# Optimization experiments

Measured on AMD Instinct MI355X. Metric: run time of the kernel, lower is better.

## Reference

```python
import jax, jax.numpy as jnp
import numpy as np

N_POINTS = 2_000_000
DIM_FEAT = 32
GRID_H, GRID_W = 1024, 1024


def setup_inputs() -> dict:
    key = jax.random.key(0)
    k1, k2 = jax.random.split(key)
    # normalized coords in [-1, 1], grid_sample convention: coord[:,0]=x (W axis), coord[:,1]=y (H axis)
    coord = jax.random.uniform(k1, (N_POINTS, 2), dtype=jnp.float32, minval=-1.0, maxval=1.0)
    # learned feature grid [1, C, H, W] (original inits zeros; use randn for a non-trivial test)
    params = jax.random.normal(k2, (1, DIM_FEAT, GRID_H, GRID_W), dtype=jnp.float32)
    return {"coord": coord, "params": params}


def _grid_sample_2d(params, coord):
    """Bilinear grid_sample, align_corners=True, border-clamped corners.

    params: [1, C, H, W]; coord: [N, 2] in [-1, 1]. Returns [N, C].
    """
    C, H, W = params.shape[1], params.shape[2], params.shape[3]
    x, y = coord[:, 0], coord[:, 1]
    # unnormalize (align_corners=True)
    ix = (x + 1.0) * 0.5 * (W - 1)
    iy = (y + 1.0) * 0.5 * (H - 1)
    ix0 = jnp.floor(ix)
    iy0 = jnp.floor(iy)
    ix1 = ix0 + 1.0
    iy1 = iy0 + 1.0
    # bilinear weights (computed before index clamping)
    w_nw = (ix1 - ix) * (iy1 - iy)
    w_ne = (ix - ix0) * (iy1 - iy)
    w_sw = (ix1 - ix) * (iy - iy0)
    w_se = (ix - ix0) * (iy - iy0)
    # clamped integer corner indices
    ix0c = jnp.clip(ix0, 0, W - 1).astype(jnp.int32)
    ix1c = jnp.clip(ix1, 0, W - 1).astype(jnp.int32)
    iy0c = jnp.clip(iy0, 0, H - 1).astype(jnp.int32)
    iy1c = jnp.clip(iy1, 0, H - 1).astype(jnp.int32)
    p = params[0]  # [C, H, W]
    # gather 4 corners -> each [C, N]
    v_nw = p[:, iy0c, ix0c]
    v_ne = p[:, iy0c, ix1c]
    v_sw = p[:, iy1c, ix0c]
    v_se = p[:, iy1c, ix1c]
    out = v_nw * w_nw + v_ne * w_ne + v_sw * w_sw + v_se * w_se  # [C, N]
    return out.T  # [N, C]


def reference(coord, params):
    return _grid_sample_2d(params, coord)
```

## Files before the change

### kernel.cpp

```cpp
#include <hip/hip_runtime.h>

constexpr int N_POINTS = 2000000;
constexpr int C = 32;
constexpr int H = 1024;
constexpr int W = 1024;

typedef float f32x4 __attribute__((ext_vector_type(4)));
typedef float f32x2 __attribute__((ext_vector_type(2)));

__global__ __launch_bounds__(256) void transpose_chw_hwc(
    const float* __restrict__ in, float* __restrict__ out)
{
    __shared__ float tile[64][C + 1];
    const int x0  = blockIdx.x * 64;
    const int y   = blockIdx.y;
    const int tid = threadIdx.x;

#pragma unroll
    for (int r = 0; r < 2; ++r) {
        const int idx = tid + 256 * r;
        const int c   = idx >> 4;
        const int xq  = idx & 15;
        const f32x4 v = __builtin_nontemporal_load(
            (const f32x4*)&in[(size_t)c * (H * W) + (size_t)y * W + x0 + xq * 4]);
        tile[xq * 4 + 0][c] = v.x;
        tile[xq * 4 + 1][c] = v.y;
        tile[xq * 4 + 2][c] = v.z;
        tile[xq * 4 + 3][c] = v.w;
    }
    __syncthreads();

#pragma unroll
    for (int r = 0; r < 2; ++r) {
        const int idx = tid + 256 * r;
        const int x   = idx >> 3;
        const int c4  = idx & 7;
        f32x4 v;
        v.x = tile[x][c4 * 4 + 0];
        v.y = tile[x][c4 * 4 + 1];
        v.z = tile[x][c4 * 4 + 2];
        v.w = tile[x][c4 * 4 + 3];
        *(f32x4*)&out[((size_t)y * W + x0 + x) * C + c4 * 4] = v;
    }
}

__global__ __launch_bounds__(256) void sample_hwc(
    const float* __restrict__ coord, const float* __restrict__ tp,
    float* __restrict__ out)
{
    const int tid = blockIdx.x * blockDim.x + threadIdx.x;
    const int n = tid >> 3;
    const int j = tid & 7;
    if (n >= N_POINTS) return;

    const f32x2 xy = __builtin_nontemporal_load(&((const f32x2*)coord)[n]);

    const float ix = (xy.x + 1.0f) * 0.5f * (float)(W - 1);
    const float iy = (xy.y + 1.0f) * 0.5f * (float)(H - 1);
    const float ix0f = floorf(ix), iy0f = floorf(iy);
    const float ix1f = ix0f + 1.0f, iy1f = iy0f + 1.0f;

    const float w_nw = (ix1f - ix) * (iy1f - iy);
    const float w_ne = (ix - ix0f) * (iy1f - iy);
    const float w_sw = (ix1f - ix) * (iy - iy0f);
    const float w_se = (ix - ix0f) * (iy - iy0f);

    const int x0 = (int)fminf(fmaxf(ix0f, 0.0f), (float)(W - 1));
    const int x1 = (int)fminf(fmaxf(ix1f, 0.0f), (float)(W - 1));
    const int y0 = (int)fminf(fmaxf(iy0f, 0.0f), (float)(H - 1));
    const int y1 = (int)fminf(fmaxf(iy1f, 0.0f), (float)(H - 1));

    const int off = j * 4;
    const f32x4 vnw = *(const f32x4*)&tp[((size_t)(y0 * W + x0)) * C + off];
    const f32x4 vne = *(const f32x4*)&tp[((size_t)(y0 * W + x1)) * C + off];
    const f32x4 vsw = *(const f32x4*)&tp[((size_t)(y1 * W + x0)) * C + off];
    const f32x4 vse = *(const f32x4*)&tp[((size_t)(y1 * W + x1)) * C + off];

    f32x4 r = vnw * w_nw + vne * w_ne + vsw * w_sw + vse * w_se;

    __builtin_nontemporal_store(r, (f32x4*)&out[(size_t)n * C + off]);
}

__global__ __launch_bounds__(256) void sample_chw(
    const float* __restrict__ coord, const float* __restrict__ p,
    float* __restrict__ out)
{
    const int tid = blockIdx.x * blockDim.x + threadIdx.x;
    const int n = tid >> 5;
    const int c = tid & 31;
    if (n >= N_POINTS) return;

    const float2 xy = ((const float2*)coord)[n];
    const float ix = (xy.x + 1.0f) * 0.5f * (float)(W - 1);
    const float iy = (xy.y + 1.0f) * 0.5f * (float)(H - 1);
    const float ix0f = floorf(ix), iy0f = floorf(iy);
    const float ix1f = ix0f + 1.0f, iy1f = iy0f + 1.0f;

    const float w_nw = (ix1f - ix) * (iy1f - iy);
    const float w_ne = (ix - ix0f) * (iy1f - iy);
    const float w_sw = (ix1f - ix) * (iy - iy0f);
    const float w_se = (ix - ix0f) * (iy - iy0f);

    const int x0 = (int)fminf(fmaxf(ix0f, 0.0f), (float)(W - 1));
    const int x1 = (int)fminf(fmaxf(ix1f, 0.0f), (float)(W - 1));
    const int y0 = (int)fminf(fmaxf(iy0f, 0.0f), (float)(H - 1));
    const int y1 = (int)fminf(fmaxf(iy1f, 0.0f), (float)(H - 1));

    const size_t plane = (size_t)c * (H * W);
    const float vnw = p[plane + (size_t)y0 * W + x0];
    const float vne = p[plane + (size_t)y0 * W + x1];
    const float vsw = p[plane + (size_t)y1 * W + x0];
    const float vse = p[plane + (size_t)y1 * W + x1];

    out[(size_t)n * C + c] = vnw * w_nw + vne * w_ne + vsw * w_sw + vse * w_se;
}

extern "C" void kernel_launch(void* const* d_in, const int* in_sizes, int n_in,
                              void* d_out, int out_size, void* d_ws, size_t ws_size,
                              hipStream_t stream)
{
    const float* coord  = (const float*)d_in[0];
    const float* params = (const float*)d_in[1];
    float* out = (float*)d_out;

    const size_t needed = (size_t)C * H * W * sizeof(float);

    if (ws_size >= needed) {
        float* tp = (float*)d_ws;
        dim3 tgrid(W / 64, H);
        transpose_chw_hwc<<<tgrid, 256, 0, stream>>>(params, tp);

        const int total = N_POINTS * 8;
        const int blocks = (total + 255) / 256;
        sample_hwc<<<blocks, 256, 0, stream>>>(coord, tp, out);
    } else {
        const int total = N_POINTS * 32;
        const int blocks = (total + 255) / 256;
        sample_chw<<<blocks, 256, 0, stream>>>(coord, params, out);
    }
}
```

Before: 491.0 us.

## Bin points by spatial tile before sampling to improve gather locality

Adds a counting-sort pipeline (zero, count with atomics, scan, scatter) that groups points into 16x16 pixel bins, then samples each bin in its own block so the corner gathers from the transposed HWC grid hit nearby memory. This aims to replace random 128-byte gathers across a 128 MB table with cache-friendly accesses. In exchange it adds several kernel launches, atomics, an extra pass over the coordinates, scattered output writes, and a larger workspace. If the workspace is too small, it falls back to the old path.

```diff
diff --git a/kernel.cpp b/kernel.cpp
--- a/kernel.cpp
+++ b/kernel.cpp
@@ -5,8 +5,32 @@
 constexpr int H = 1024;
 constexpr int W = 1024;
 
+constexpr int BIN_SHIFT = 4;
+constexpr int BINS_X = W >> BIN_SHIFT;
+constexpr int BINS_Y = H >> BIN_SHIFT;
+constexpr int N_BINS = BINS_X * BINS_Y;
+
 typedef float f32x4 __attribute__((ext_vector_type(4)));
 typedef float f32x2 __attribute__((ext_vector_type(2)));
+
+constexpr size_t TP_BYTES   = (size_t)H * W * C * sizeof(float);
+constexpr size_t OFS_COUNTS = TP_BYTES;
+constexpr size_t OFS_START  = TP_BYTES + 32768;
+constexpr size_t OFS_CURSOR = TP_BYTES + 65536;
+constexpr size_t OFS_SIDX   = TP_BYTES + 98304;
+constexpr size_t OFS_SCOORD = OFS_SIDX + (size_t)N_POINTS * sizeof(int);
+constexpr size_t WS_NEEDED  = OFS_SCOORD + (size_t)N_POINTS * 2 * sizeof(float);
+
+__device__ __forceinline__ int point_bin(float x, float y)
+{
+    const float ix = (x + 1.0f) * 0.5f * (float)(W - 1);
+    const float iy = (y + 1.0f) * 0.5f * (float)(H - 1);
+    int bx = ((int)ix) >> BIN_SHIFT;
+    int by = ((int)iy) >> BIN_SHIFT;
+    bx = max(0, min(bx, BINS_X - 1));
+    by = max(0, min(by, BINS_Y - 1));
+    return by * BINS_X + bx;
+}
 
 __global__ __launch_bounds__(256) void transpose_chw_hwc(
     const float* __restrict__ in, float* __restrict__ out)
@@ -44,6 +68,107 @@
     }
 }
 
+__global__ __launch_bounds__(256) void zero_bins(int* __restrict__ counts)
+{
+    const int i = blockIdx.x * 256 + threadIdx.x;
+    if (i < N_BINS) counts[i] = 0;
+}
+
+__global__ __launch_bounds__(256) void count_points(
+    const float* __restrict__ coord, int* __restrict__ counts)
+{
+    const int stride = gridDim.x * 256;
+    for (int n = blockIdx.x * 256 + threadIdx.x; n < N_POINTS; n += stride) {
+        const f32x2 xy = ((const f32x2*)coord)[n];
+        atomicAdd(&counts[point_bin(xy.x, xy.y)], 1);
+    }
+}
+
+__global__ __launch_bounds__(256) void scan_bins(
+    const int* __restrict__ counts, int* __restrict__ binStart,
+    int* __restrict__ cursor)
+{
+    __shared__ int part[256];
+    const int t = threadIdx.x;
+    int local[16];
+    int sum = 0;
+#pragma unroll
+    for (int k = 0; k < 16; ++k) { local[k] = counts[t * 16 + k]; sum += local[k]; }
+    part[t] = sum;
+    __syncthreads();
+    for (int off = 1; off < 256; off <<= 1) {
+        const int v = (t >= off) ? part[t - off] : 0;
+        __syncthreads();
+        part[t] += v;
+        __syncthreads();
+    }
+    int run = part[t] - sum;
+#pragma unroll
+    for (int k = 0; k < 16; ++k) {
+        const int b = t * 16 + k;
+        binStart[b] = run;
+        cursor[b]   = run;
+        run += local[k];
+    }
+    if (t == 255) binStart[N_BINS] = run;
+}
+
+__global__ __launch_bounds__(256) void scatter_points(
+    const float* __restrict__ coord, int* __restrict__ cursor,
+    int* __restrict__ sortedIdx, f32x2* __restrict__ sortedCoord)
+{
+    const int stride = gridDim.x * 256;
+    for (int n = blockIdx.x * 256 + threadIdx.x; n < N_POINTS; n += stride) {
+        const f32x2 xy = ((const f32x2*)coord)[n];
+        int pos = atomicAdd(&cursor[point_bin(xy.x, xy.y)], 1);
+        pos = max(0, min(pos, N_POINTS - 1));
+        sortedIdx[pos]   = n;
+        sortedCoord[pos] = xy;
+    }
+}
+
+__global__ __launch_bounds__(256) void sample_binned(
+    const f32x2* __restrict__ sortedCoord, const int* __restrict__ sortedIdx,
+    const int* __restrict__ binStart, const float* __restrict__ tp,
+    float* __restrict__ out)
+{
+    const int b     = blockIdx.x;
+    const int start = binStart[b];
+    const int end   = binStart[b + 1];
+    const int tid   = threadIdx.x;
+    const int j     = tid & 7;
+    const int off   = j * 4;
+
+    for (int i = start + (tid >> 3); i < end; i += 32) {
+        const f32x2 xy = sortedCoord[i];
+        const int   n  = sortedIdx[i];
+        if ((unsigned)n >= (unsigned)N_POINTS) continue;
+
+        const float ix = (xy.x + 1.0f) * 0.5f * (float)(W - 1);
+        const float iy = (xy.y + 1.0f) * 0.5f * (float)(H - 1);
+        const float ix0f = floorf(ix), iy0f = floorf(iy);
+        const float ix1f = ix0f + 1.0f, iy1f = iy0f + 1.0f;
+
+        const float w_nw = (ix1f - ix) * (iy1f - iy);
+        const float w_ne = (ix - ix0f) * (iy1f - iy);
+        const float w_sw = (ix1f - ix) * (iy - iy0f);
+        const float w_se = (ix - ix0f) * (iy - iy0f);
+
+        const int x0 = (int)fminf(fmaxf(ix0f, 0.0f), (float)(W - 1));
+        const int x1 = (int)fminf(fmaxf(ix1f, 0.0f), (float)(W - 1));
+        const int y0 = (int)fminf(fmaxf(iy0f, 0.0f), (float)(H - 1));
+        const int y1 = (int)fminf(fmaxf(iy1f, 0.0f), (float)(H - 1));
+
+        const f32x4 vnw = *(const f32x4*)&tp[((size_t)(y0 * W + x0)) * C + off];
+        const f32x4 vne = *(const f32x4*)&tp[((size_t)(y0 * W + x1)) * C + off];
+        const f32x4 vsw = *(const f32x4*)&tp[((size_t)(y1 * W + x0)) * C + off];
+        const f32x4 vse = *(const f32x4*)&tp[((size_t)(y1 * W + x1)) * C + off];
+
+        const f32x4 r = vnw * w_nw + vne * w_ne + vsw * w_sw + vse * w_se;
+        __builtin_nontemporal_store(r, (f32x4*)&out[(size_t)n * C + off]);
+    }
+}
+
 __global__ __launch_bounds__(256) void sample_hwc(
     const float* __restrict__ coord, const float* __restrict__ tp,
     float* __restrict__ out)
@@ -53,8 +178,7 @@
     const int j = tid & 7;
     if (n >= N_POINTS) return;
 
-    const f32x2 xy = __builtin_nontemporal_load(&((const f32x2*)coord)[n]);
-
+    const f32x2 xy = ((const f32x2*)coord)[n];
     const float ix = (xy.x + 1.0f) * 0.5f * (float)(W - 1);
     const float iy = (xy.y + 1.0f) * 0.5f * (float)(H - 1);
     const float ix0f = floorf(ix), iy0f = floorf(iy);
@@ -76,8 +200,7 @@
     const f32x4 vsw = *(const f32x4*)&tp[((size_t)(y1 * W + x0)) * C + off];
     const f32x4 vse = *(const f32x4*)&tp[((size_t)(y1 * W + x1)) * C + off];
 
-    f32x4 r = vnw * w_nw + vne * w_ne + vsw * w_sw + vse * w_se;
-
+    const f32x4 r = vnw * w_nw + vne * w_ne + vsw * w_sw + vse * w_se;
     __builtin_nontemporal_store(r, (f32x4*)&out[(size_t)n * C + off]);
 }
 
@@ -123,19 +246,31 @@
     const float* params = (const float*)d_in[1];
     float* out = (float*)d_out;
 
-    const size_t needed = (size_t)C * H * W * sizeof(float);
-
-    if (ws_size >= needed) {
-        float* tp = (float*)d_ws;
+    char* ws = (char*)d_ws;
+
+    if (ws_size >= WS_NEEDED) {
+        float* tp          = (float*)(ws);
+        int*   counts      = (int*)(ws + OFS_COUNTS);
+        int*   binStart    = (int*)(ws + OFS_START);
+        int*   cursor      = (int*)(ws + OFS_CURSOR);
+        int*   sortedIdx   = (int*)(ws + OFS_SIDX);
+        f32x2* sortedCoord = (f32x2*)(ws + OFS_SCOORD);
+
+        zero_bins<<<(N_BINS + 255) / 256, 256, 0, stream>>>(counts);
         dim3 tgrid(W / 64, H);
         transpose_chw_hwc<<<tgrid, 256, 0, stream>>>(params, tp);
-
-        const int total = N_POINTS * 8;
-        const int blocks = (total + 255) / 256;
+        count_points<<<2048, 256, 0, stream>>>(coord, counts);
+        scan_bins<<<1, 256, 0, stream>>>(counts, binStart, cursor);
+        scatter_points<<<2048, 256, 0, stream>>>(coord, cursor, sortedIdx, sortedCoord);
+        sample_binned<<<N_BINS, 256, 0, stream>>>(sortedCoord, sortedIdx, binStart, tp, out);
+    } else if (ws_size >= TP_BYTES) {
+        float* tp = (float*)ws;
+        dim3 tgrid(W / 64, H);
+        transpose_chw_hwc<<<tgrid, 256, 0, stream>>>(params, tp);
+        const int blocks = (N_POINTS * 8 + 255) / 256;
         sample_hwc<<<blocks, 256, 0, stream>>>(coord, tp, out);
     } else {
-        const int total = N_POINTS * 32;
-        const int blocks = (total + 255) / 256;
+        const int blocks = (N_POINTS * 32 + 255) / 256;
         sample_chw<<<blocks, 256, 0, stream>>>(coord, params, out);
     }
 }
```

After: 713.8 us. +45.4%, slower.
